# Performance work log

Measured on AMD Instinct MI355X. Metric: run time of the kernel, lower is better.

The kernel has to match this reference:

```python
import jax, jax.numpy as jnp
import numpy as np

G, N_REAL, C_IN, C_EDGE, H, D, C_EOUT = 4096, 31, 64, 64, 4, 64, 64
N_NODE = N_REAL + 1  # 32, last local node is the supernode


def setup_inputs() -> dict:
    key = jax.random.key(0)
    # per-graph edge template: bidirectional ring over real nodes (consecutive (u,v),(v,u) pairs),
    # then edges (u, supernode)
    u = np.arange(N_REAL)
    v = (u + 1) % N_REAL
    ring_src = np.stack([u, v], 1).reshape(-1)
    ring_dst = np.stack([v, u], 1).reshape(-1)
    ls = np.concatenate([ring_src, np.arange(N_REAL)])
    ld = np.concatenate([ring_dst, np.full(N_REAL, N_REAL)])
    Eg = ls.shape[0]  # 93
    off = np.arange(G) * N_NODE
    edge_index = np.stack([(off[:, None] + ls[None, :]).reshape(-1),
                           (off[:, None] + ld[None, :]).reshape(-1)])
    N = G * N_NODE
    E = G * Eg
    k1, k2, k3, k4, k5 = jax.random.split(key, 5)
    return {
        "x": jax.random.normal(k1, (N, C_IN), jnp.float32),
        "edge_index": jnp.asarray(edge_index, jnp.int32),
        "edge_inform": jax.random.normal(k2, (E, C_EDGE), jnp.float32) * 0.1,
        "batch": jnp.asarray(np.repeat(np.arange(G), N_NODE), jnp.int32),
        "edge_num": jnp.asarray(np.full(G, Eg), jnp.int32),
        "W_lin_l": jax.random.normal(k3, (C_IN + C_EDGE, H * D), jnp.float32) * 0.05,
        "att_l": jax.random.normal(k4, (1, H, D), jnp.float32) * 0.1,
        "bias": jnp.zeros((D,), jnp.float32),
        "W_ec": jax.random.normal(k5, (C_EDGE, C_EOUT), jnp.float32) * 0.1,
        "b_ec": jnp.zeros((C_EOUT,), jnp.float32),
    }


def reference(x, edge_index, edge_inform, batch, edge_num, W_lin_l, att_l, bias, W_ec, b_ec):
    # graph structure is static metadata -> numpy
    ei = np.asarray(edge_index)
    en = np.asarray(edge_num)
    N = x.shape[0]
    G_ = en.shape[0]
    Eg = int(en[0])
    n = N // G_
    src = jnp.asarray(ei[0])
    dst = jnp.asarray(ei[1])
    Hh, Dd = att_l.shape[1], att_l.shape[2]

    # degree counting (the per-edge python loop in the original)
    deg = jnp.zeros((N,), x.dtype).at[dst].add(1.0)

    # GAT-style edge attention + scatter-sum
    h = jnp.concatenate([x[src], edge_inform], axis=1) @ W_lin_l  # [E, H*D]
    h = h.reshape(-1, Hh, Dd)
    alpha = jax.nn.leaky_relu(jnp.sum(h * att_l, axis=-1))  # [E,H], slope 0.01
    amax = jax.ops.segment_max(alpha, dst, num_segments=N)
    ex = jnp.exp(alpha - amax[dst])
    a = ex / (jax.ops.segment_sum(ex, dst, num_segments=N)[dst] + 1e-16)
    xi = jax.ops.segment_sum(h * a[..., None], dst, num_segments=N)  # [N,H,D]
    out = xi.mean(axis=1) + bias

    # per-graph edge aggregation (structure uniform across graphs by construction)
    le = ei.reshape(2, G_, Eg) - (np.arange(G_) * n)[None, :, None]
    l0, l1 = le[0, 0], le[1, 0]  # local template indices, same for every graph
    midx = np.nonzero((l1 != n - 1) & (l0 != l1))[0]  # mask: drop supernode-dst & self-loops
    even = midx[0::2]
    C = edge_inform.shape[1]
    inf_g = edge_inform.reshape(G_, Eg, C)

    mdst = jnp.asarray(l1[midx])
    eisum = jax.vmap(lambda v: jax.ops.segment_sum(v, mdst, num_segments=n - 1))(inf_g[:, midx])  # [G,n-1,C]

    es, ed = l0[even], l1[even]
    deg_g = deg.reshape(G_, n)
    norm = deg_g[:, es] + deg_g[:, ed] - 2.0  # edge_norm; divide by edge_norm - 1
    temp = (eisum[:, es] + eisum[:, ed] - inf_g[:, even]) / (norm - 1.0)[..., None]  # [G,P,C]
    temps2 = jnp.repeat(temp, 2, axis=1)  # each temp appended twice

    l1_all = jnp.asarray(l1)
    cnt = jnp.zeros((n,), x.dtype).at[l1_all].add(1.0)
    esum_all = jax.vmap(lambda v: jax.ops.segment_sum(v, l1_all, num_segments=n))(inf_g)
    emean = esum_all / cnt[None, :, None]  # scatter reduce='mean'

    gather = jnp.concatenate([temps2, emean, emean[:, : n - 1]], axis=1).reshape(-1, C)
    new_edge_inform = jax.nn.leaky_relu(gather @ W_ec + b_ec)
    return out, new_edge_inform
```

## Files before the change

### kernel.cpp

```cpp
#include <hip/hip_runtime.h>
#include <hip/hip_fp16.h>

#define NUM_G 4096
#define RS 72
#define OUT2_OFF ((size_t)NUM_G * 32 * 64)

typedef _Float16 half8  __attribute__((ext_vector_type(8)));
typedef _Float16 half4v __attribute__((ext_vector_type(4)));
typedef float    floatx4 __attribute__((ext_vector_type(4)));

__device__ __forceinline__ float lrelu(float v) { return v > 0.f ? v : 0.01f * v; }

__global__ void setup_prep(const float* __restrict__ W, const float* __restrict__ att,
                           const float* __restrict__ Wec,
                           _Float16* __restrict__ vp16, _Float16* __restrict__ BT,
                           _Float16* __restrict__ BT2)
{
    const int t = threadIdx.x, b = blockIdx.x;
    if (b == 0) {
        for (int i = t; i < 1024; i += 256) {
            const int h8 = i >> 6, k = i & 63;
            float acc = 0.f;
            if (h8 < 8) {
                const int h = h8 & 3, ro = (h8 < 4) ? 0 : 64;
                for (int d = 0; d < 64; ++d) acc += W[(ro + k) * 256 + h * 64 + d] * att[h * 64 + d];
            }
            vp16[i] = (_Float16)acc;
        }
    }
    for (int i = b * 4096 + t; i < (b + 1) * 4096; i += 256) {
        const int d = i >> 9, kk = i & 511, h = kk >> 7, k = kk & 127;
        BT[i] = (_Float16)W[k * 256 + h * 64 + d];
    }
    for (int i = b * 512 + t; i < b * 512 + 512; i += 256) {
        const int d = i >> 6, k = i & 63;
        BT2[i] = (_Float16)Wec[k * 64 + d];
    }
}

__global__ __launch_bounds__(256, 4) void fused_main(
    const float* __restrict__ x, const float* __restrict__ einf,
    const float* __restrict__ bias, const float* __restrict__ bec,
    const _Float16* __restrict__ vp16, const _Float16* __restrict__ BT,
    const _Float16* __restrict__ BT2,
    float* __restrict__ out, float* __restrict__ out2)
{
    __shared__ __align__(16) _Float16 R[128 * RS];
    __shared__ __align__(16) _Float16 A2[64 * RS];
    __shared__ __align__(16) float    sal[128 * 9];
    __shared__ __align__(16) float    al4[93 * 4];
    __shared__ __align__(16) _Float16 virt[512];

    const int t = threadIdx.x;
    const int g = blockIdx.x;
    const int lane = t & 63;
    const int w = t >> 6;
    const int m16 = lane & 15, q = lane >> 4;

    {
        const float4* xg4 = (const float4*)(x + (size_t)g * 2048);
        for (int i = t; i < 512; i += 256) {
            float4 v = xg4[i];
            half4v h4 = {(_Float16)v.x, (_Float16)v.y, (_Float16)v.z, (_Float16)v.w};
            *(half4v*)(R + (i >> 4) * RS + (i & 15) * 4) = h4;
        }
        const float4* eg4 = (const float4*)(einf + (size_t)g * 5952);
        for (int i = t; i < 1488; i += 256) {
            float4 v = eg4[i];
            half4v h4 = {(_Float16)v.x, (_Float16)v.y, (_Float16)v.z, (_Float16)v.w};
            *(half4v*)(R + (32 + (i >> 4)) * RS + (i & 15) * 4) = h4;
        }
        if (t < 27) {
            half8 z = {0, 0, 0, 0, 0, 0, 0, 0};
            *(half8*)(R + 125 * RS + t * 8) = z;
        }
    }
    half8 bF0 = *(const half8*)(vp16 + m16 * 64 + q * 8);
    half8 bF1 = *(const half8*)(vp16 + m16 * 64 + 32 + q * 8);
    __syncthreads();

    #pragma unroll
    for (int j = 0; j < 2; ++j) {
        const int tile = w * 2 + j;
        const _Float16* arow = R + (tile * 16 + m16) * RS;
        half8 aF0 = *(const half8*)(arow + q * 8);
        half8 aF1 = *(const half8*)(arow + 32 + q * 8);
        floatx4 s = {0.f, 0.f, 0.f, 0.f};
        s = __builtin_amdgcn_mfma_f32_16x16x32_f16(aF0, bF0, s, 0, 0, 0);
        s = __builtin_amdgcn_mfma_f32_16x16x32_f16(aF1, bF1, s, 0, 0, 0);
        if (m16 < 8) {
            #pragma unroll
            for (int r = 0; r < 4; ++r)
                sal[(tile * 16 + q * 4 + r) * 9 + m16] = s[r];
        }
    }
    __syncthreads();

    if (t < 128) {
        const int n = t >> 2, h = t & 3;
        if (n < 31) {
            const int s1 = (n + 30) % 31, s2 = (n + 1) % 31;
            const int e1 = 2 * s1, e2 = 2 * n + 1;
            const float a1 = lrelu(sal[s1 * 9 + h] + sal[(32 + e1) * 9 + 4 + h]);
            const float a2 = lrelu(sal[s2 * 9 + h] + sal[(32 + e2) * 9 + 4 + h]);
            const float m = fmaxf(a1, a2);
            const float x1 = __expf(a1 - m), x2 = __expf(a2 - m);
            const float inv = 1.f / (x1 + x2 + 1e-16f);
            al4[e1 * 4 + h] = x1 * inv;
            al4[e2 * 4 + h] = x2 * inv;
        } else {
            float m = -1e30f;
            for (int i = 0; i < 31; ++i)
                m = fmaxf(m, lrelu(sal[i * 9 + h] + sal[(94 + i) * 9 + 4 + h]));
            float sden = 1e-16f;
            for (int i = 0; i < 31; ++i)
                sden += __expf(lrelu(sal[i * 9 + h] + sal[(94 + i) * 9 + 4 + h]) - m);
            const float inv = 1.f / sden;
            for (int i = 0; i < 31; ++i)
                al4[(62 + i) * 4 + h] =
                    __expf(lrelu(sal[i * 9 + h] + sal[(94 + i) * 9 + 4 + h]) - m) * inv;
        }
    } else {
        const _Float16* E = R + 32 * RS;
        for (int idx = t - 128; idx < 992; idx += 128) {
            const int r = idx >> 4, c = (idx & 15) * 4;
            half4v v;
            if (r < 31) {
                const int ra = 2 * ((r + 30) % 31), rb = 2 * r + 1, rc = 2 * ((r + 1) % 31) + 1;
                v = *(const half4v*)(E + ra * RS + c) + *(const half4v*)(E + rb * RS + c)
                  + *(const half4v*)(E + rc * RS + c);
            } else {
                const int jj = r - 31;
                const int ra = 2 * ((jj + 30) % 31), rb = 2 * jj + 1;
                v = (*(const half4v*)(E + ra * RS + c) + *(const half4v*)(E + rb * RS + c))
                    * (_Float16)0.5f;
            }
            *(half4v*)(A2 + r * RS + c) = v;
        }
        if (t < 192) {
            const int c = t - 128;
            float s = 0.f;
            for (int i = 0; i < 31; ++i) s += (float)E[(62 + i) * RS + c];
            A2[62 * RS + c] = (_Float16)(s * (1.f / 31.f));
        } else {
            A2[63 * RS + (t - 192)] = (_Float16)0.f;
        }
    }
    __syncthreads();

    {
        const int hf = w >> 1;
        const int base = hf ? 94 : 0;
        half8 aV;
        #pragma unroll
        for (int j = 0; j < 8; ++j) {
            const int i = q * 8 + j;
            aV[j] = (m16 < 4 && i < 31) ? (_Float16)al4[(62 + i) * 4 + m16] : (_Float16)0.f;
        }
        #pragma unroll
        for (int u = 0; u < 2; ++u) {
            const int nt = (w & 1) * 2 + u;
            half8 bV;
            #pragma unroll
            for (int j = 0; j < 8; ++j) {
                const int i = q * 8 + j;
                bV[j] = (i < 31) ? R[(base + i) * RS + nt * 16 + m16] : (_Float16)0.f;
            }
            floatx4 vc = {0.f, 0.f, 0.f, 0.f};
            vc = __builtin_amdgcn_mfma_f32_16x16x32_f16(aV, bV, vc, 0, 0, 0);
            if (q == 0) {
                #pragma unroll
                for (int r = 0; r < 4; ++r)
                    virt[r * 128 + hf * 64 + nt * 16 + m16] = (_Float16)vc[r];
            }
        }
    }
    __syncthreads();

    const int co = w * 16 + m16;
    half8 b2a = *(const half8*)(BT2 + co * 64 + q * 8);
    half8 b2b = *(const half8*)(BT2 + co * 64 + 32 + q * 8);

    {
        const int n1c = (16 + m16 < 31) ? 16 + m16 : 30;
        const int s1_0 = (m16 + 30) % 31, s2_0 = (m16 + 1) % 31;
        const int e1_0 = 2 * s1_0, e2_0 = 2 * m16 + 1;
        const int s1_1 = (n1c + 30) % 31, s2_1 = (n1c + 1) % 31;
        const int e1_1 = 2 * s1_1, e2_1 = 2 * n1c + 1;
        _Float16 a1_0[4], a2_0[4], a1_1[4], a2_1[4];
        #pragma unroll
        for (int h = 0; h < 4; ++h) {
            a1_0[h] = (_Float16)al4[e1_0 * 4 + h];
            a2_0[h] = (_Float16)al4[e2_0 * 4 + h];
            a1_1[h] = (_Float16)al4[e1_1 * 4 + h];
            a2_1[h] = (_Float16)al4[e2_1 * 4 + h];
        }
        floatx4 acc0 = {0.f, 0.f, 0.f, 0.f}, acc1 = {0.f, 0.f, 0.f, 0.f};
        #pragma unroll
        for (int hf = 0; hf < 2; ++hf) {
            const int rA0 = hf ? 32 + e1_0 : s1_0, rB0 = hf ? 32 + e2_0 : s2_0;
            const int rA1 = hf ? 32 + e1_1 : s1_1, rB1 = hf ? 32 + e2_1 : s2_1;
            #pragma unroll
            for (int kc = 0; kc < 2; ++kc) {
                const int k0 = kc * 32 + q * 8;
                half8 x1 = *(const half8*)(R + rA0 * RS + k0);
                half8 x2 = *(const half8*)(R + rB0 * RS + k0);
                half8 y1 = *(const half8*)(R + rA1 * RS + k0);
                half8 y2 = *(const half8*)(R + rB1 * RS + k0);
                #pragma unroll
                for (int h = 0; h < 4; ++h) {
                    half8 b = *(const half8*)(BT + co * 512 + h * 128 + hf * 64 + k0);
                    half8 af0 = x1 * a1_0[h] + x2 * a2_0[h];
                    acc0 = __builtin_amdgcn_mfma_f32_16x16x32_f16(af0, b, acc0, 0, 0, 0);
                    half8 af1 = y1 * a1_1[h] + y2 * a2_1[h];
                    half8 vv = *(const half8*)(virt + h * 128 + hf * 64 + k0);
                    af1 = (m16 == 15) ? vv : af1;
                    acc1 = __builtin_amdgcn_mfma_f32_16x16x32_f16(af1, b, acc1, 0, 0, 0);
                }
            }
        }
        const float bv = bias[co];
        float* og = out + (size_t)g * 2048;
        #pragma unroll
        for (int r = 0; r < 4; ++r) {
            og[(q * 4 + r) * 64 + co]        = 0.25f * acc0[r] + bv;
            og[(16 + q * 4 + r) * 64 + co]   = 0.25f * acc1[r] + bv;
        }
    }

    {
        floatx4 z = {0.f, 0.f, 0.f, 0.f};
        floatx4 acc2[4]; acc2[0] = z; acc2[1] = z; acc2[2] = z; acc2[3] = z;
        #pragma unroll
        for (int kk = 0; kk < 2; ++kk) {
            half8 b = kk ? b2b : b2a;
            #pragma unroll
            for (int mt = 0; mt < 4; ++mt) {
                half8 a = *(const half8*)(A2 + (mt * 16 + m16) * RS + kk * 32 + q * 8);
                acc2[mt] = __builtin_amdgcn_mfma_f32_16x16x32_f16(a, b, acc2[mt], 0, 0, 0);
            }
        }
        const float bv2 = bec[co];
        float* o2 = out2 + (size_t)g * 8000;
        #pragma unroll
        for (int mt = 0; mt < 4; ++mt) {
            #pragma unroll
            for (int r = 0; r < 4; ++r) {
                const int row = mt * 16 + q * 4 + r;
                if (row >= 63) continue;
                const float v = lrelu(acc2[mt][r] + bv2);
                if (row < 31) {
                    o2[(2 * row) * 64 + co]     = v;
                    o2[(2 * row + 1) * 64 + co] = v;
                } else if (row < 62) {
                    o2[(62 + row - 31) * 64 + co] = v;
                    o2[(94 + row - 31) * 64 + co] = v;
                } else {
                    o2[93 * 64 + co] = v;
                }
            }
        }
    }
}

extern "C" void kernel_launch(void* const* d_in, const int* in_sizes, int n_in,
                              void* d_out, int out_size, void* d_ws, size_t ws_size,
                              hipStream_t stream) {
    const float* x    = (const float*)d_in[0];
    const float* einf = (const float*)d_in[2];
    const float* W    = (const float*)d_in[5];
    const float* att  = (const float*)d_in[6];
    const float* bias = (const float*)d_in[7];
    const float* Wec  = (const float*)d_in[8];
    const float* bec  = (const float*)d_in[9];
    float* out  = (float*)d_out;
    float* out2 = out + OUT2_OFF;

    _Float16* vp16 = (_Float16*)d_ws;
    _Float16* BT   = (_Float16*)((char*)d_ws + 2048);
    _Float16* BT2  = (_Float16*)((char*)d_ws + 2048 + 65536);

    setup_prep<<<8, 256, 0, stream>>>(W, att, Wec, vp16, BT, BT2);
    fused_main<<<NUM_G, 256, 0, stream>>>(x, einf, bias, bec, vp16, BT, BT2, out, out2);
}
```

Measured before the change: 323.1 us.

## Swizzle LDS layout, parallelize supernode softmax, drop a barrier, raise occupancy

Replaces the padded row stride with an XOR-swizzled 64-wide layout, shrinking shared memory so more blocks fit per CU, and raises the launch-bounds occupancy hint from 4 to 5. The serial per-head supernode softmax now runs in one wave using shuffle reductions. That wave also computes the virtual-node MFMA right away, so one block-wide barrier is removed. Attention weights are stored as fp16, which lets them be loaded as a vector, at a small precision cost. The risks are register pressure under the tighter launch bounds, and wave 0 becoming the critical path because it now does all of the virtual-node work.

```diff
diff --git a/kernel.cpp b/kernel.cpp
--- a/kernel.cpp
+++ b/kernel.cpp
@@ -2,7 +2,6 @@
 #include <hip/hip_fp16.h>
 
 #define NUM_G 4096
-#define RS 72
 #define OUT2_OFF ((size_t)NUM_G * 32 * 64)
 
 typedef _Float16 half8  __attribute__((ext_vector_type(8)));
@@ -10,6 +9,10 @@
 typedef float    floatx4 __attribute__((ext_vector_type(4)));
 
 __device__ __forceinline__ float lrelu(float v) { return v > 0.f ? v : 0.01f * v; }
+
+__device__ __forceinline__ int swz(int row, int col) {
+    return row * 64 + (col ^ ((row & 7) << 3));
+}
 
 __global__ void setup_prep(const float* __restrict__ W, const float* __restrict__ att,
                            const float* __restrict__ Wec,
@@ -38,17 +41,17 @@
     }
 }
 
-__global__ __launch_bounds__(256, 4) void fused_main(
+__global__ __launch_bounds__(256, 5) void fused_main(
     const float* __restrict__ x, const float* __restrict__ einf,
     const float* __restrict__ bias, const float* __restrict__ bec,
     const _Float16* __restrict__ vp16, const _Float16* __restrict__ BT,
     const _Float16* __restrict__ BT2,
     float* __restrict__ out, float* __restrict__ out2)
 {
-    __shared__ __align__(16) _Float16 R[128 * RS];
-    __shared__ __align__(16) _Float16 A2[64 * RS];
+    __shared__ __align__(16) _Float16 R[128 * 64];
+    __shared__ __align__(16) _Float16 A2[64 * 64];
     __shared__ __align__(16) float    sal[128 * 9];
-    __shared__ __align__(16) float    al4[93 * 4];
+    __shared__ __align__(16) _Float16 al4h[96 * 4];
     __shared__ __align__(16) _Float16 virt[512];
 
     const int t = threadIdx.x;
@@ -62,17 +65,17 @@
         for (int i = t; i < 512; i += 256) {
             float4 v = xg4[i];
             half4v h4 = {(_Float16)v.x, (_Float16)v.y, (_Float16)v.z, (_Float16)v.w};
-            *(half4v*)(R + (i >> 4) * RS + (i & 15) * 4) = h4;
+            *(half4v*)(R + swz(i >> 4, (i & 15) * 4)) = h4;
         }
         const float4* eg4 = (const float4*)(einf + (size_t)g * 5952);
         for (int i = t; i < 1488; i += 256) {
             float4 v = eg4[i];
             half4v h4 = {(_Float16)v.x, (_Float16)v.y, (_Float16)v.z, (_Float16)v.w};
-            *(half4v*)(R + (32 + (i >> 4)) * RS + (i & 15) * 4) = h4;
-        }
-        if (t < 27) {
+            *(half4v*)(R + swz(32 + (i >> 4), (i & 15) * 4)) = h4;
+        }
+        if (t < 24) {
             half8 z = {0, 0, 0, 0, 0, 0, 0, 0};
-            *(half8*)(R + 125 * RS + t * 8) = z;
+            *(half8*)(R + 125 * 64 + t * 8) = z;
         }
     }
     half8 bF0 = *(const half8*)(vp16 + m16 * 64 + q * 8);
@@ -82,9 +85,9 @@
     #pragma unroll
     for (int j = 0; j < 2; ++j) {
         const int tile = w * 2 + j;
-        const _Float16* arow = R + (tile * 16 + m16) * RS;
-        half8 aF0 = *(const half8*)(arow + q * 8);
-        half8 aF1 = *(const half8*)(arow + 32 + q * 8);
+        const int row = tile * 16 + m16;
+        half8 aF0 = *(const half8*)(R + swz(row, q * 8));
+        half8 aF1 = *(const half8*)(R + swz(row, 32 + q * 8));
         floatx4 s = {0.f, 0.f, 0.f, 0.f};
         s = __builtin_amdgcn_mfma_f32_16x16x32_f16(aF0, bF0, s, 0, 0, 0);
         s = __builtin_amdgcn_mfma_f32_16x16x32_f16(aF1, bF1, s, 0, 0, 0);
@@ -96,83 +99,102 @@
     }
     __syncthreads();
 
-    if (t < 128) {
-        const int n = t >> 2, h = t & 3;
-        if (n < 31) {
-            const int s1 = (n + 30) % 31, s2 = (n + 1) % 31;
-            const int e1 = 2 * s1, e2 = 2 * n + 1;
-            const float a1 = lrelu(sal[s1 * 9 + h] + sal[(32 + e1) * 9 + 4 + h]);
-            const float a2 = lrelu(sal[s2 * 9 + h] + sal[(32 + e2) * 9 + 4 + h]);
-            const float m = fmaxf(a1, a2);
-            const float x1 = __expf(a1 - m), x2 = __expf(a2 - m);
-            const float inv = 1.f / (x1 + x2 + 1e-16f);
-            al4[e1 * 4 + h] = x1 * inv;
-            al4[e2 * 4 + h] = x2 * inv;
-        } else {
-            float m = -1e30f;
-            for (int i = 0; i < 31; ++i)
-                m = fmaxf(m, lrelu(sal[i * 9 + h] + sal[(94 + i) * 9 + 4 + h]));
-            float sden = 1e-16f;
-            for (int i = 0; i < 31; ++i)
-                sden += __expf(lrelu(sal[i * 9 + h] + sal[(94 + i) * 9 + 4 + h]) - m);
-            const float inv = 1.f / sden;
-            for (int i = 0; i < 31; ++i)
-                al4[(62 + i) * 4 + h] =
-                    __expf(lrelu(sal[i * 9 + h] + sal[(94 + i) * 9 + 4 + h]) - m) * inv;
+    if (w == 0) {
+        const int i = lane;
+        const bool act = (i < 31);
+        float av[4], mx[4], wv[4];
+        #pragma unroll
+        for (int h = 0; h < 4; ++h)
+            av[h] = act ? lrelu(sal[i * 9 + h] + sal[(94 + i) * 9 + 4 + h]) : -1e30f;
+        #pragma unroll
+        for (int h = 0; h < 4; ++h) {
+            float m = av[h];
+            #pragma unroll
+            for (int off = 32; off > 0; off >>= 1)
+                m = fmaxf(m, __shfl_xor(m, off, 64));
+            mx[h] = m;
+        }
+        #pragma unroll
+        for (int h = 0; h < 4; ++h) {
+            float e = act ? __expf(av[h] - mx[h]) : 0.f;
+            float s = e;
+            #pragma unroll
+            for (int off = 32; off > 0; off >>= 1)
+                s += __shfl_xor(s, off, 64);
+            wv[h] = e / (s + 1e-16f);
+        }
+        if (act) {
+            half4v hv = {(_Float16)wv[0], (_Float16)wv[1], (_Float16)wv[2], (_Float16)wv[3]};
+            *(half4v*)(al4h + (62 + i) * 4) = hv;
+        }
+        asm volatile("s_waitcnt lgkmcnt(0)" ::: "memory");
+        __builtin_amdgcn_wave_barrier();
+        half8 aV;
+        #pragma unroll
+        for (int j = 0; j < 8; ++j) {
+            const int e = q * 8 + j;
+            aV[j] = (m16 < 4 && e < 31) ? al4h[(62 + e) * 4 + m16] : (_Float16)0.f;
+        }
+        #pragma unroll
+        for (int hf = 0; hf < 2; ++hf) {
+            const int base = hf ? 94 : 0;
+            #pragma unroll
+            for (int nt = 0; nt < 4; ++nt) {
+                half8 bV;
+                #pragma unroll
+                for (int j = 0; j < 8; ++j) {
+                    const int e = q * 8 + j;
+                    bV[j] = (e < 31) ? R[swz(base + e, nt * 16 + m16)] : (_Float16)0.f;
+                }
+                floatx4 vc = {0.f, 0.f, 0.f, 0.f};
+                vc = __builtin_amdgcn_mfma_f32_16x16x32_f16(aV, bV, vc, 0, 0, 0);
+                if (q == 0) {
+                    #pragma unroll
+                    for (int r = 0; r < 4; ++r)
+                        virt[r * 128 + hf * 64 + nt * 16 + m16] = (_Float16)vc[r];
+                }
+            }
+        }
+    } else if (w == 1) {
+        #pragma unroll
+        for (int rep = 0; rep < 2; ++rep) {
+            const int item = lane * 2 + rep;
+            if (item < 124) {
+                const int n = item >> 2, h = item & 3;
+                const int s1 = (n + 30) % 31, s2 = (n + 1) % 31;
+                const int e1 = 2 * s1, e2 = 2 * n + 1;
+                const float a1 = lrelu(sal[s1 * 9 + h] + sal[(32 + e1) * 9 + 4 + h]);
+                const float a2 = lrelu(sal[s2 * 9 + h] + sal[(32 + e2) * 9 + 4 + h]);
+                const float m = fmaxf(a1, a2);
+                const float x1 = __expf(a1 - m), x2 = __expf(a2 - m);
+                const float inv = 1.f / (x1 + x2 + 1e-16f);
+                al4h[e1 * 4 + h] = (_Float16)(x1 * inv);
+                al4h[e2 * 4 + h] = (_Float16)(x2 * inv);
+            }
         }
     } else {
-        const _Float16* E = R + 32 * RS;
         for (int idx = t - 128; idx < 992; idx += 128) {
             const int r = idx >> 4, c = (idx & 15) * 4;
             half4v v;
             if (r < 31) {
                 const int ra = 2 * ((r + 30) % 31), rb = 2 * r + 1, rc = 2 * ((r + 1) % 31) + 1;
-                v = *(const half4v*)(E + ra * RS + c) + *(const half4v*)(E + rb * RS + c)
-                  + *(const half4v*)(E + rc * RS + c);
+                v = *(const half4v*)(R + swz(32 + ra, c)) + *(const half4v*)(R + swz(32 + rb, c))
+                  + *(const half4v*)(R + swz(32 + rc, c));
             } else {
                 const int jj = r - 31;
                 const int ra = 2 * ((jj + 30) % 31), rb = 2 * jj + 1;
-                v = (*(const half4v*)(E + ra * RS + c) + *(const half4v*)(E + rb * RS + c))
+                v = (*(const half4v*)(R + swz(32 + ra, c)) + *(const half4v*)(R + swz(32 + rb, c)))
                     * (_Float16)0.5f;
             }
-            *(half4v*)(A2 + r * RS + c) = v;
+            *(half4v*)(A2 + swz(r, c)) = v;
         }
         if (t < 192) {
             const int c = t - 128;
             float s = 0.f;
-            for (int i = 0; i < 31; ++i) s += (float)E[(62 + i) * RS + c];
-            A2[62 * RS + c] = (_Float16)(s * (1.f / 31.f));
+            for (int i = 0; i < 31; ++i) s += (float)R[swz(94 + i, c)];
+            A2[swz(62, c)] = (_Float16)(s * (1.f / 31.f));
         } else {
-            A2[63 * RS + (t - 192)] = (_Float16)0.f;
-        }
-    }
-    __syncthreads();
-
-    {
-        const int hf = w >> 1;
-        const int base = hf ? 94 : 0;
-        half8 aV;
-        #pragma unroll
-        for (int j = 0; j < 8; ++j) {
-            const int i = q * 8 + j;
-            aV[j] = (m16 < 4 && i < 31) ? (_Float16)al4[(62 + i) * 4 + m16] : (_Float16)0.f;
-        }
-        #pragma unroll
-        for (int u = 0; u < 2; ++u) {
-            const int nt = (w & 1) * 2 + u;
-            half8 bV;
-            #pragma unroll
-            for (int j = 0; j < 8; ++j) {
-                const int i = q * 8 + j;
-                bV[j] = (i < 31) ? R[(base + i) * RS + nt * 16 + m16] : (_Float16)0.f;
-            }
-            floatx4 vc = {0.f, 0.f, 0.f, 0.f};
-            vc = __builtin_amdgcn_mfma_f32_16x16x32_f16(aV, bV, vc, 0, 0, 0);
-            if (q == 0) {
-                #pragma unroll
-                for (int r = 0; r < 4; ++r)
-                    virt[r * 128 + hf * 64 + nt * 16 + m16] = (_Float16)vc[r];
-            }
+            A2[swz(63, t - 192)] = (_Float16)0.f;
         }
     }
     __syncthreads();
@@ -187,14 +209,10 @@
         const int e1_0 = 2 * s1_0, e2_0 = 2 * m16 + 1;
         const int s1_1 = (n1c + 30) % 31, s2_1 = (n1c + 1) % 31;
         const int e1_1 = 2 * s1_1, e2_1 = 2 * n1c + 1;
-        _Float16 a1_0[4], a2_0[4], a1_1[4], a2_1[4];
-        #pragma unroll
-        for (int h = 0; h < 4; ++h) {
-            a1_0[h] = (_Float16)al4[e1_0 * 4 + h];
-            a2_0[h] = (_Float16)al4[e2_0 * 4 + h];
-            a1_1[h] = (_Float16)al4[e1_1 * 4 + h];
-            a2_1[h] = (_Float16)al4[e2_1 * 4 + h];
-        }
+        half4v a1_0 = *(const half4v*)(al4h + e1_0 * 4);
+        half4v a2_0 = *(const half4v*)(al4h + e2_0 * 4);
+        half4v a1_1 = *(const half4v*)(al4h + e1_1 * 4);
+        half4v a2_1 = *(const half4v*)(al4h + e2_1 * 4);
         floatx4 acc0 = {0.f, 0.f, 0.f, 0.f}, acc1 = {0.f, 0.f, 0.f, 0.f};
         #pragma unroll
         for (int hf = 0; hf < 2; ++hf) {
@@ -203,10 +221,10 @@
             #pragma unroll
             for (int kc = 0; kc < 2; ++kc) {
                 const int k0 = kc * 32 + q * 8;
-                half8 x1 = *(const half8*)(R + rA0 * RS + k0);
-                half8 x2 = *(const half8*)(R + rB0 * RS + k0);
-                half8 y1 = *(const half8*)(R + rA1 * RS + k0);
-                half8 y2 = *(const half8*)(R + rB1 * RS + k0);
+                half8 x1 = *(const half8*)(R + swz(rA0, k0));
+                half8 x2 = *(const half8*)(R + swz(rB0, k0));
+                half8 y1 = *(const half8*)(R + swz(rA1, k0));
+                half8 y2 = *(const half8*)(R + swz(rB1, k0));
                 #pragma unroll
                 for (int h = 0; h < 4; ++h) {
                     half8 b = *(const half8*)(BT + co * 512 + h * 128 + hf * 64 + k0);
@@ -236,7 +254,7 @@
             half8 b = kk ? b2b : b2a;
             #pragma unroll
             for (int mt = 0; mt < 4; ++mt) {
-                half8 a = *(const half8*)(A2 + (mt * 16 + m16) * RS + kk * 32 + q * 8);
+                half8 a = *(const half8*)(A2 + swz(mt * 16 + m16, kk * 32 + q * 8));
                 acc2[mt] = __builtin_amdgcn_mfma_f32_16x16x32_f16(a, b, acc2[mt], 0, 0, 0);
             }
         }
```

Measured after the change: 323.2 us. Within noise of the previous version (+0.0%).
